# Performance work log

Hardware: AMD Instinct MI355X
Metric: run time of the kernel (lower is better)

The kernel has to match this reference:

```python
import jax, jax.numpy as jnp
import numpy as np

MA_K = 2 * 125 + 1  # 251, moving-average kernel
MV_K = 4 * 125 + 1  # 501, moving-variance kernel
EPS = 1e-5


def _avg_pool1d(x, K):
    """PyTorch F.avg_pool1d(stride=1, padding=(K-1)//2, count_include_pad=True)
    computed in O(L) via prefix sums. x: (B, C, L) -> (B, C, L)."""
    pad = (K - 1) // 2
    xp = jnp.pad(x, ((0, 0), (0, 0), (pad, pad)))  # zero pad, length L+K-1
    c = jnp.pad(jnp.cumsum(xp, axis=-1), ((0, 0), (0, 0), (1, 0)))  # length L+K
    return (c[..., K:] - c[..., :-K]) / K  # divide by K always (count_include_pad)


def setup_inputs() -> dict:
    key = jax.random.key(0)
    x = jax.random.normal(key, (8192, 1, 3750), dtype=jnp.float32)
    return {"x": x}


def reference(x):
    # global z-norm per (batch, channel); torch.std is unbiased (ddof=1)
    x = (x - jnp.mean(x, axis=2, keepdims=True)) / (
        jnp.std(x, axis=2, keepdims=True, ddof=1) + EPS)
    # remove moving average (kernel 251)
    x = x - _avg_pool1d(x, MA_K)
    # rescale by moving std (kernel 501)
    x = x / (jnp.sqrt(_avg_pool1d(x * x, MV_K)) + EPS)
    return x
```

## Files before the change

kernel.cpp:

```cpp
#include <hip/hip_runtime.h>
#include <math.h>

namespace {

constexpr int L      = 3750;
constexpr int NPAIR  = L / 2;
constexpr int BLK    = 256;
constexpr int CH     = 15;
constexpr int NCHUNK = L / CH;
constexpr float EPS  = 1e-5f;

__device__ __forceinline__ float frcp(float x)  { return __builtin_amdgcn_rcpf(x); }
__device__ __forceinline__ float fsqrt(float x) { return __builtin_amdgcn_sqrtf(x); }

__global__ __launch_bounds__(BLK, 8)
void preproc_kernel(const float* __restrict__ in, float* __restrict__ out) {
    __shared__ __align__(16) float sp[L + 2];
    __shared__ float sred[8];

    const int tid  = threadIdx.x;
    const int lane = tid & 63;
    const int wave = tid >> 6;
    const size_t rowoff = (size_t)blockIdx.x * (size_t)L;
    const float* rin  = in  + rowoff;
    float*       rout = out + rowoff;

    const bool active = (tid < NCHUNK);
    const int  base   = tid * CH;

    {
        const float2* rin2 = reinterpret_cast<const float2*>(rin);
        float2* sp2 = reinterpret_cast<float2*>(sp);
        for (int i = tid; i < NPAIR; i += BLK) sp2[i] = rin2[i];
    }
    __syncthreads();

    float y[CH];
    float cy = 0.f, cy2 = 0.f;
    if (active) {
        #pragma unroll
        for (int j = 0; j < CH; ++j) {
            const float v = sp[base + j];
            y[j] = v;
            cy  += v;
            cy2  = fmaf(v, v, cy2);
        }
    } else {
        #pragma unroll
        for (int j = 0; j < CH; ++j) y[j] = 0.f;
    }
    float iy = cy;
    #pragma unroll
    for (int d = 1; d < 64; d <<= 1) {
        const float u = __shfl_up(iy, (unsigned)d, 64);
        if (lane >= d) iy += u;
    }
    float t2 = cy2;
    #pragma unroll
    for (int d = 1; d < 64; d <<= 1) t2 += __shfl_xor(t2, d, 64);
    if (lane == 63) { sred[wave] = iy; sred[4 + wave] = t2; }
    __syncthreads();
    float woff = 0.f;
    #pragma unroll
    for (int w = 0; w < 4; ++w) if (w < wave) woff += sred[w];
    const float totY  = sred[0] + sred[1] + sred[2] + sred[3];
    const float totY2 = sred[4] + sred[5] + sred[6] + sred[7];
    const float mean  = totY * (1.f / (float)L);
    const float var   = (totY2 - totY * mean) * (1.f / (float)(L - 1));
    const float s     = fsqrt(var) + EPS;
    const float epsS  = EPS * s;

    {
        float run = woff + iy - cy;
        if (active) {
            #pragma unroll
            for (int j = 0; j < CH; ++j) { sp[base + j] = run; run += y[j]; }
            if (tid == NCHUNK - 1) sp[L] = run;
        }
    }
    __syncthreads();

    const float inv251 = 1.f / 251.f;
    float cu = 0.f;
    if (active) {
        if (tid >= 9 && tid <= 240) {
            #pragma unroll
            for (int j = 0; j < CH; ++j) {
                const int i = base + j;
                const float sumY = sp[i + 126] - sp[i - 125];
                const float u = fmaf(sumY, -inv251, y[j]);
                y[j] = u;
                cu   = fmaf(u, u, cu);
            }
        } else {
            #pragma unroll
            for (int j = 0; j < CH; ++j) {
                const int i  = base + j;
                const int lo = (i > 125) ? i - 125 : 0;
                const int hi = (i + 126 < L) ? i + 126 : L;
                const float sumY = sp[hi] - sp[lo];
                const float cnt  = (float)(hi - lo);
                float u = y[j] - mean * (1.f - cnt * inv251);
                u = fmaf(sumY, -inv251, u);
                y[j] = u;
                cu   = fmaf(u, u, cu);
            }
        }
    }
    float iu = cu;
    #pragma unroll
    for (int d = 1; d < 64; d <<= 1) {
        const float u = __shfl_up(iu, (unsigned)d, 64);
        if (lane >= d) iu += u;
    }
    if (lane == 63) sred[wave] = iu;
    __syncthreads();
    float woff2 = 0.f;
    #pragma unroll
    for (int w = 0; w < 4; ++w) if (w < wave) woff2 += sred[w];

    {
        float run = woff2 + iu - cu;
        if (active) {
            #pragma unroll
            for (int j = 0; j < CH; ++j) { sp[base + j] = run; run = fmaf(y[j], y[j], run); }
            if (tid == NCHUNK - 1) sp[L] = run;
        }
    }
    __syncthreads();

    const float inv501 = 1.f / 501.f;
    if (active) {
        if (tid >= 17 && tid <= 232) {
            #pragma unroll
            for (int j = 0; j < CH; ++j) {
                const int i = base + j;
                float W = (sp[i + 251] - sp[i - 250]) * inv501;
                W = fmaxf(W, 0.f);
                y[j] = y[j] * frcp(fsqrt(W) + epsS);
            }
        } else {
            #pragma unroll
            for (int j = 0; j < CH; ++j) {
                const int i  = base + j;
                const int lo = (i > 250) ? i - 250 : 0;
                const int hi = (i + 251 < L) ? i + 251 : L;
                float W = (sp[hi] - sp[lo]) * inv501;
                W = fmaxf(W, 0.f);
                y[j] = y[j] * frcp(fsqrt(W) + epsS);
            }
        }
    }
    __syncthreads();

    if (active) {
        #pragma unroll
        for (int j = 0; j < CH; ++j) sp[base + j] = y[j];
    }
    __syncthreads();

    {
        const float2* sp2 = reinterpret_cast<const float2*>(sp);
        float2* rout2 = reinterpret_cast<float2*>(rout);
        for (int i = tid; i < NPAIR; i += BLK) rout2[i] = sp2[i];
    }
}

}

extern "C" void kernel_launch(void* const* d_in, const int* in_sizes, int n_in,
                              void* d_out, int out_size, void* d_ws, size_t ws_size,
                              hipStream_t stream) {
    const float* x = (const float*)d_in[0];
    float* out = (float*)d_out;
    const int rows = in_sizes[0] / L;
    preproc_kernel<<<rows, BLK, 0, stream>>>(x, out);
}
```

Measured before the change: 48.33 us.

## Halve block size, double per-thread chunk, vectorize LDS accesses as float2

Switches from 256 threads with 15 elements each to 128 threads with 30 elements each, so the block has two waves and the cross-wave scan offsets shrink to a single conditional. LDS loads and stores of the per-thread chunk, and the aligned side of each window difference, now use float2 accesses to cut LDS instruction count. The interior-thread bounds for the 251 and 501 windows are recomputed for the new chunk size. The cost is more registers per thread (launch bounds lowered) and fewer threads to hide latency per block.

Measured after the change: 66.55 us. 1.38x slower.

```diff
diff --git a/kernel.cpp b/kernel.cpp
--- a/kernel.cpp
+++ b/kernel.cpp
@@ -5,18 +5,18 @@
 
 constexpr int L      = 3750;
 constexpr int NPAIR  = L / 2;
-constexpr int BLK    = 256;
-constexpr int CH     = 15;
+constexpr int BLK    = 128;
+constexpr int CH     = 30;
 constexpr int NCHUNK = L / CH;
 constexpr float EPS  = 1e-5f;
 
 __device__ __forceinline__ float frcp(float x)  { return __builtin_amdgcn_rcpf(x); }
 __device__ __forceinline__ float fsqrt(float x) { return __builtin_amdgcn_sqrtf(x); }
 
-__global__ __launch_bounds__(BLK, 8)
+__global__ __launch_bounds__(BLK, 5)
 void preproc_kernel(const float* __restrict__ in, float* __restrict__ out) {
     __shared__ __align__(16) float sp[L + 2];
-    __shared__ float sred[8];
+    __shared__ float sred[4];
 
     const int tid  = threadIdx.x;
     const int lane = tid & 63;
@@ -38,12 +38,15 @@
     float y[CH];
     float cy = 0.f, cy2 = 0.f;
     if (active) {
-        #pragma unroll
-        for (int j = 0; j < CH; ++j) {
-            const float v = sp[base + j];
-            y[j] = v;
-            cy  += v;
-            cy2  = fmaf(v, v, cy2);
+        const float2* s2 = reinterpret_cast<const float2*>(sp) + 15 * tid;
+        #pragma unroll
+        for (int h = 0; h < 15; ++h) {
+            const float2 v = s2[h];
+            y[2*h]   = v.x;
+            y[2*h+1] = v.y;
+            cy  += v.x + v.y;
+            cy2  = fmaf(v.x, v.x, cy2);
+            cy2  = fmaf(v.y, v.y, cy2);
         }
     } else {
         #pragma unroll
@@ -58,39 +61,47 @@
     float t2 = cy2;
     #pragma unroll
     for (int d = 1; d < 64; d <<= 1) t2 += __shfl_xor(t2, d, 64);
-    if (lane == 63) { sred[wave] = iy; sred[4 + wave] = t2; }
-    __syncthreads();
-    float woff = 0.f;
-    #pragma unroll
-    for (int w = 0; w < 4; ++w) if (w < wave) woff += sred[w];
-    const float totY  = sred[0] + sred[1] + sred[2] + sred[3];
-    const float totY2 = sred[4] + sred[5] + sred[6] + sred[7];
+    if (lane == 63) { sred[wave] = iy; sred[2 + wave] = t2; }
+    __syncthreads();
+    const float woff  = (wave == 1) ? sred[0] : 0.f;
+    const float totY  = sred[0] + sred[1];
+    const float totY2 = sred[2] + sred[3];
     const float mean  = totY * (1.f / (float)L);
     const float var   = (totY2 - totY * mean) * (1.f / (float)(L - 1));
     const float s     = fsqrt(var) + EPS;
     const float epsS  = EPS * s;
 
-    {
+    if (active) {
         float run = woff + iy - cy;
-        if (active) {
-            #pragma unroll
-            for (int j = 0; j < CH; ++j) { sp[base + j] = run; run += y[j]; }
-            if (tid == NCHUNK - 1) sp[L] = run;
-        }
+        float2* w2 = reinterpret_cast<float2*>(sp) + 15 * tid;
+        #pragma unroll
+        for (int h = 0; h < 15; ++h) {
+            float2 w;
+            w.x = run; run += y[2*h];
+            w.y = run; run += y[2*h+1];
+            w2[h] = w;
+        }
+        if (tid == NCHUNK - 1) sp[L] = run;
     }
     __syncthreads();
 
     const float inv251 = 1.f / 251.f;
     float cu = 0.f;
     if (active) {
-        if (tid >= 9 && tid <= 240) {
-            #pragma unroll
-            for (int j = 0; j < CH; ++j) {
-                const int i = base + j;
-                const float sumY = sp[i + 126] - sp[i - 125];
-                const float u = fmaf(sumY, -inv251, y[j]);
-                y[j] = u;
-                cu   = fmaf(u, u, cu);
+        if (tid >= 5 && tid <= 119) {
+            const float2* hi2 = reinterpret_cast<const float2*>(sp) + 15 * tid + 63;
+            const float*  pl  = sp + base - 125;
+            #pragma unroll
+            for (int h = 0; h < 15; ++h) {
+                const float2 hi = hi2[h];
+                const float lo0 = pl[2*h];
+                const float lo1 = pl[2*h+1];
+                float u0 = fmaf(hi.x - lo0, -inv251, y[2*h]);
+                float u1 = fmaf(hi.y - lo1, -inv251, y[2*h+1]);
+                y[2*h]   = u0;
+                y[2*h+1] = u1;
+                cu = fmaf(u0, u0, cu);
+                cu = fmaf(u1, u1, cu);
             }
         } else {
             #pragma unroll
@@ -115,29 +126,38 @@
     }
     if (lane == 63) sred[wave] = iu;
     __syncthreads();
-    float woff2 = 0.f;
-    #pragma unroll
-    for (int w = 0; w < 4; ++w) if (w < wave) woff2 += sred[w];
-
-    {
+    const float woff2 = (wave == 1) ? sred[0] : 0.f;
+
+    if (active) {
         float run = woff2 + iu - cu;
-        if (active) {
-            #pragma unroll
-            for (int j = 0; j < CH; ++j) { sp[base + j] = run; run = fmaf(y[j], y[j], run); }
-            if (tid == NCHUNK - 1) sp[L] = run;
-        }
+        float2* w2 = reinterpret_cast<float2*>(sp) + 15 * tid;
+        #pragma unroll
+        for (int h = 0; h < 15; ++h) {
+            float2 w;
+            w.x = run; run = fmaf(y[2*h],   y[2*h],   run);
+            w.y = run; run = fmaf(y[2*h+1], y[2*h+1], run);
+            w2[h] = w;
+        }
+        if (tid == NCHUNK - 1) sp[L] = run;
     }
     __syncthreads();
 
     const float inv501 = 1.f / 501.f;
     if (active) {
-        if (tid >= 17 && tid <= 232) {
-            #pragma unroll
-            for (int j = 0; j < CH; ++j) {
-                const int i = base + j;
-                float W = (sp[i + 251] - sp[i - 250]) * inv501;
-                W = fmaxf(W, 0.f);
-                y[j] = y[j] * frcp(fsqrt(W) + epsS);
+        if (tid >= 9 && tid <= 115) {
+            const float2* lo2 = reinterpret_cast<const float2*>(sp) + 15 * tid - 125;
+            const float*  ph  = sp + base + 251;
+            #pragma unroll
+            for (int h = 0; h < 15; ++h) {
+                const float2 lo = lo2[h];
+                const float hi0 = ph[2*h];
+                const float hi1 = ph[2*h+1];
+                float W0 = (hi0 - lo.x) * inv501;
+                float W1 = (hi1 - lo.y) * inv501;
+                W0 = fmaxf(W0, 0.f);
+                W1 = fmaxf(W1, 0.f);
+                y[2*h]   = y[2*h]   * frcp(fsqrt(W0) + epsS);
+                y[2*h+1] = y[2*h+1] * frcp(fsqrt(W1) + epsS);
             }
         } else {
             #pragma unroll
@@ -154,8 +174,14 @@
     __syncthreads();
 
     if (active) {
-        #pragma unroll
-        for (int j = 0; j < CH; ++j) sp[base + j] = y[j];
+        float2* w2 = reinterpret_cast<float2*>(sp) + 15 * tid;
+        #pragma unroll
+        for (int h = 0; h < 15; ++h) {
+            float2 v;
+            v.x = y[2*h];
+            v.y = y[2*h+1];
+            w2[h] = v;
+        }
     }
     __syncthreads();
 
```
